# Optimization experiments

Measured on AMD Instinct MI355X. Metric: run time of the kernel, lower is better.

The kernel has to match this reference:

```python
import jax, jax.numpy as jnp
import numpy as np

B, S, T = 1024, 1024, 16


def setup_inputs() -> dict:
    key = jax.random.key(0)
    k1, k2, k3, k4, k5 = jax.random.split(key, 5)
    emissions = jax.random.normal(k1, (B, S, T), dtype=jnp.float32)
    tags = jax.random.randint(k2, (B, S), 0, T, dtype=jnp.int64)
    mask = jnp.ones((B, S), dtype=bool)
    # parameters (original uses uniform(-0.1, 0.1) init)
    transitions = jax.random.uniform(k3, (T, T), minval=-0.1, maxval=0.1, dtype=jnp.float32)
    start_transitions = jax.random.uniform(k4, (T,), minval=-0.1, maxval=0.1, dtype=jnp.float32)
    end_transitions = jax.random.uniform(k5, (T,), minval=-0.1, maxval=0.1, dtype=jnp.float32)
    return {
        "emissions": emissions,
        "tags": tags,
        "mask": mask,
        "transitions": transitions,
        "start_transitions": start_transitions,
        "end_transitions": end_transitions,
    }


def _forward_algorithm(emissions, mask, transitions, start_transitions, end_transitions):
    # emissions: [B,S,T], mask: [B,S] bool -> log partition [B]
    score0 = start_transitions + emissions[:, 0]  # [B,T]

    def step(score, xs):
        em_t, m_t = xs  # em_t: [B,T], m_t: [B]
        # next[b,i,j] = score[b,i] + transitions[i,j] + em_t[b,j]
        nxt = score[:, :, None] + transitions[None, :, :] + em_t[:, None, :]
        nxt = jax.nn.logsumexp(nxt, axis=1)  # over previous tag i
        score = jnp.where(m_t[:, None], nxt, score)
        return score, None

    em_rest = jnp.swapaxes(emissions[:, 1:], 0, 1)  # [S-1,B,T]
    m_rest = jnp.swapaxes(mask[:, 1:], 0, 1)        # [S-1,B]
    score, _ = jax.lax.scan(step, score0, (em_rest, m_rest))
    score = score + end_transitions
    return jax.nn.logsumexp(score, axis=1)


def _score_sentence(emissions, tags, mask, transitions, start_transitions, end_transitions):
    # gold-path score, vectorized over time. [B]
    bidx = jnp.arange(emissions.shape[0])
    score = start_transitions[tags[:, 0]] + emissions[:, 0][bidx, tags[:, 0]]
    # per-step emission scores [B,S]
    emit = jnp.take_along_axis(emissions, tags[:, :, None], axis=2)[:, :, 0]
    # NOTE: faithful to original: transitions[tags[t], tags[t-1]]
    trans = transitions[tags[:, 1:], tags[:, :-1]]  # [B,S-1]
    m = mask[:, 1:].astype(emissions.dtype)
    score = score + jnp.sum((emit[:, 1:] + trans) * m, axis=1)
    last_idx = jnp.sum(mask.astype(jnp.int32), axis=1) - 1  # [B]
    last_tags = jnp.take_along_axis(tags, last_idx[:, None].astype(tags.dtype), axis=1)[:, 0]
    score = score + end_transitions[last_tags]
    return score


def reference(emissions, tags, mask, transitions, start_transitions, end_transitions):
    emissions = emissions.astype(jnp.float32)
    gold = _score_sentence(emissions, tags, mask, transitions, start_transitions, end_transitions)
    logZ = _forward_algorithm(emissions, mask, transitions, start_transitions, end_transitions)
    nll = logZ - gold
    return jnp.mean(nll)
```

## Files before the change

### kernel.cpp

```cpp
#include <hip/hip_runtime.h>
#include <stdint.h>


#define BB 1024
#define SS 1024
#define TT 16
#define CC 16
#define LL 64
#define XS 68
#define P1B (BB * CC / 4)

typedef float    f32x4 __attribute__((ext_vector_type(4)));
typedef float    f32x2 __attribute__((ext_vector_type(2)));
typedef int      i32x4 __attribute__((ext_vector_type(4)));
typedef short    s16x4 __attribute__((ext_vector_type(4)));
typedef uint32_t u32x2 __attribute__((ext_vector_type(2)));

__device__ __forceinline__ uint32_t pkt(float lo, float hi) {
    return __builtin_amdgcn_perm(__float_as_uint(hi), __float_as_uint(lo), 0x07060302u);
}
__device__ __forceinline__ s16x4 mk_frag(uint32_t lo, uint32_t hi) {
    u32x2 t; t.x = lo; t.y = hi;
    return __builtin_bit_cast(s16x4, t);
}

__global__ __launch_bounds__(256, 4) void fused1_kernel(
        const float* __restrict__ em,
        const float* __restrict__ trans,
        const int*   __restrict__ tags,
        const float* __restrict__ startt,
        const float* __restrict__ endt,
        float* __restrict__ mats,
        int*   __restrict__ scales,
        float* __restrict__ gold,
        float* __restrict__ out)
{
    __shared__ float xbuf[4][TT * XS];
    __shared__ int   sbuf[4][16];
    __shared__ float red[256];
    if (blockIdx.x < P1B) {
        const int wave = threadIdx.x >> 6;
        const int lane = threadIdx.x & 63;
        const int id   = blockIdx.x * 4 + wave;
        const int b    = id >> 4;
        const int c    = id & 15;
        const int q    = lane >> 4;
        const int m    = lane & 15;

        const float comp = 1.00390625f;
        f32x2 e01, e23;
        e01.x = __expf(trans[(4*q + 0) * TT + m]) * comp;
        e01.y = __expf(trans[(4*q + 1) * TT + m]) * comp;
        e23.x = __expf(trans[(4*q + 2) * TT + m]) * comp;
        e23.y = __expf(trans[(4*q + 3) * TT + m]) * comp;

        const float* ep = em + (size_t)b * SS * TT + (size_t)c * LL * TT + lane;
        float* xb = xbuf[wave];
        {
            float v[16];
            #pragma unroll
            for (int k = 0; k < 16; ++k) v[k] = ep[k * 64];
            #pragma unroll
            for (int k = 0; k < 16; ++k) xb[m * XS + 4 * k + q] = __expf(v[k]);
        }

        f32x4 sd0, sd1;
        sd0[0] = sd1[0] = (4*q + 0 == m) ? 1.f : 0.f;
        sd0[1] = sd1[1] = (4*q + 1 == m) ? 1.f : 0.f;
        sd0[2] = sd1[2] = (4*q + 2 == m) ? 1.f : 0.f;
        sd0[3] = sd1[3] = (4*q + 3 == m) ? 1.f : 0.f;
        const f32x4 zero = {0.f, 0.f, 0.f, 0.f};
        int sc0 = 0, sc1 = 0;
        const bool skip0 = (c == 0);

#define RESCALE(sd, sc) {                                                   \
        float mx = fmaxf(fmaxf(sd[0], sd[1]), fmaxf(sd[2], sd[3]));         \
        mx = fmaxf(mx, __shfl_xor(mx, 16, 64));                             \
        mx = fmaxf(mx, __shfl_xor(mx, 32, 64));                             \
        const int e_ = (int)(__float_as_uint(mx) >> 23) - 127;              \
        const float sf_ = __uint_as_float((uint32_t)(127 - e_) << 23);      \
        sd[0] *= sf_; sd[1] *= sf_; sd[2] *= sf_; sd[3] *= sf_;             \
        sc += e_; }

#define STEP(sd, xm) {                                                      \
        f32x2 xx; xx.x = (xm); xx.y = (xm);                                 \
        const f32x2 a01 = xx * e01;                                         \
        const f32x2 a23 = xx * e23;                                         \
        const s16x4 afr = mk_frag(pkt(a01.x, a01.y), pkt(a23.x, a23.y));    \
        const s16x4 bfr = mk_frag(pkt(sd[0], sd[1]), pkt(sd[2], sd[3]));    \
        sd = __builtin_amdgcn_mfma_f32_16x16x16bf16_1k(afr, bfr, zero, 0, 0, 0); }

        const float* xrow = xb + m * XS;
        f32x4 cx0 = *(const f32x4*)(xrow);
        f32x4 cx1 = *(const f32x4*)(xrow + 32);

        #pragma unroll
        for (int g = 0; g < 8; ++g) {
            f32x4 nx0, nx1;
            if (g < 7) {
                nx0 = *(const f32x4*)(xrow + 4 * (g + 1));
                nx1 = *(const f32x4*)(xrow + 32 + 4 * (g + 1));
            }
            #pragma unroll
            for (int i = 0; i < 4; ++i) {
                if (!(skip0 && g == 0 && i == 0)) STEP(sd0, cx0[i]);
                STEP(sd1, cx1[i]);
            }
            if (g & 1) { RESCALE(sd0, sc0); RESCALE(sd1, sc1); }
            cx0 = nx0; cx1 = nx1;
        }

        xb[(4*q + 0) * TT + m] = sd1[0];
        xb[(4*q + 1) * TT + m] = sd1[1];
        xb[(4*q + 2) * TT + m] = sd1[2];
        xb[(4*q + 3) * TT + m] = sd1[3];
        if (q == 0) sbuf[wave][m] = sc1;
        const f32x4 at  = *(const f32x4*)(xb + m * TT + 4 * q);
        const i32x4 sh  = *(const i32x4*)(sbuf[wave] + 4 * q);
        int shimax = sc1;
        #pragma unroll
        for (int s = 1; s < 16; s <<= 1) shimax = max(shimax, __shfl_xor(shimax, s, 64));
        const float r0 = ldexpf(sd0[0], sh.x - shimax);
        const float r1 = ldexpf(sd0[1], sh.y - shimax);
        const float r2 = ldexpf(sd0[2], sh.z - shimax);
        const float r3 = ldexpf(sd0[3], sh.w - shimax);
        const s16x4 bfm = mk_frag(pkt(r0, r1), pkt(r2, r3));
        const s16x4 afm = mk_frag(pkt(at.x, at.y), pkt(at.z, at.w));
        f32x4 sd = __builtin_amdgcn_mfma_f32_16x16x16bf16_1k(afm, bfm, zero, 0, 0, 0);
        int sc = sc0 + shimax;
        RESCALE(sd, sc);
#undef RESCALE
#undef STEP

        float* mp = mats + (size_t)id * 256;
        mp[(4*q + 0) * TT + m] = sd[0];
        mp[(4*q + 1) * TT + m] = sd[1];
        mp[(4*q + 2) * TT + m] = sd[2];
        mp[(4*q + 3) * TT + m] = sd[3];
        if (q == 0) scales[id * 16 + m] = sc;
    } else {
        const int b = blockIdx.x - P1B, tid = threadIdx.x;
        if (b == 0 && tid == 0) out[0] = 0.f;
        float local = 0.f;
        for (int t = tid; t < SS; t += 256) {
            const int tg = tags[b * SS + t];
            float v = em[(size_t)(b * SS + t) * TT + tg];
            if (t > 0) v += trans[tg * TT + tags[b * SS + t - 1]];
            else       v += startt[tg];
            if (t == SS - 1) v += endt[tg];
            local += v;
        }
        red[tid] = local; __syncthreads();
        for (int s = 128; s > 0; s >>= 1) { if (tid < s) red[tid] += red[tid + s]; __syncthreads(); }
        if (tid == 0) gold[b] = red[0];
    }
}

__global__ __launch_bounds__(256) void combine_kernel(
        const float* __restrict__ em,
        const float* __restrict__ startt,
        const float* __restrict__ endt,
        const float* __restrict__ mats,
        const int*   __restrict__ scales,
        const float* __restrict__ gold,
        float* __restrict__ out)
{
    const int wave = threadIdx.x >> 6;
    const int lane = threadIdx.x & 63;
    const int b    = blockIdx.x * 4 + wave;
    const int q    = lane >> 4;
    const int m    = lane & 15;

    const float* m0 = mats + (size_t)(b * CC) * 256;
    f32x4 d;
    d[0] = m0[(4*q + 0) * TT + m];
    d[1] = m0[(4*q + 1) * TT + m];
    d[2] = m0[(4*q + 2) * TT + m];
    d[3] = m0[(4*q + 3) * TT + m];
    int sig = scales[(b * CC) * 16 + m];
    int gam = 0;
    const f32x4 zero = {0.f, 0.f, 0.f, 0.f};

    #pragma unroll 4
    for (int c = 1; c < CC; ++c) {
        const int idc = b * CC + c;
        const f32x4 a = *(const f32x4*)(mats + (size_t)idc * 256 + m * TT + 4 * q);
        const i32x4 s = *(const i32x4*)(scales + idc * 16 + 4 * q);
        int sm = max(max(s.x, s.y), max(s.z, s.w));
        sm = max(sm, __shfl_xor(sm, 16, 64));
        sm = max(sm, __shfl_xor(sm, 32, 64));
        const float r0 = ldexpf(d[0], s.x - sm);
        const float r1 = ldexpf(d[1], s.y - sm);
        const float r2 = ldexpf(d[2], s.z - sm);
        const float r3 = ldexpf(d[3], s.w - sm);
        const s16x4 bfr = mk_frag(pkt(r0, r1), pkt(r2, r3));
        const s16x4 afr = mk_frag(pkt(a.x, a.y), pkt(a.z, a.w));
        d = __builtin_amdgcn_mfma_f32_16x16x16bf16_1k(afr, bfr, zero, 0, 0, 0);
        gam += sm;
        float mx = fmaxf(fmaxf(d[0], d[1]), fmaxf(d[2], d[3]));
        mx = fmaxf(mx, __shfl_xor(mx, 16, 64));
        mx = fmaxf(mx, __shfl_xor(mx, 32, 64));
        const int e = (int)(__float_as_uint(mx) >> 23) - 127;
        const float sf = __uint_as_float((uint32_t)(127 - e) << 23);
        d[0] *= sf; d[1] *= sf; d[2] *= sf; d[3] *= sf;
        sig += e;
    }

    const float s0 = startt[m] + em[(size_t)b * SS * TT + m];
    float mx0 = s0;
    #pragma unroll
    for (int s = 1; s < 16; s <<= 1) mx0 = fmaxf(mx0, __shfl_xor(mx0, s, 64));
    const float u0n = __expf(s0 - mx0);

    int sigmax = sig;
    #pragma unroll
    for (int s = 1; s < 16; s <<= 1) sigmax = max(sigmax, __shfl_xor(sigmax, s, 64));
    const float w = ldexpf(u0n, sig - sigmax);

    f32x4 v;
    v[0] = d[0] * w; v[1] = d[1] * w; v[2] = d[2] * w; v[3] = d[3] * w;
    #pragma unroll
    for (int s = 1; s < 16; s <<= 1) {
        v[0] += __shfl_xor(v[0], s, 64);
        v[1] += __shfl_xor(v[1], s, 64);
        v[2] += __shfl_xor(v[2], s, 64);
        v[3] += __shfl_xor(v[3], s, 64);
    }
    const f32x4 ee = *(const f32x4*)(endt + 4 * q);
    float z = __expf(ee.x) * v[0] + __expf(ee.y) * v[1]
            + __expf(ee.z) * v[2] + __expf(ee.w) * v[3];
    z += __shfl_xor(z, 16, 64);
    z += __shfl_xor(z, 32, 64);

    if (lane == 0) {
        const float logZ = mx0 + 0.69314718055994531f * (float)(gam + sigmax) + __logf(z);
        atomicAdd(out, (logZ - gold[b]) * (1.0f / BB));
    }
}

extern "C" void kernel_launch(void* const* d_in, const int* in_sizes, int n_in,
                              void* d_out, int out_size, void* d_ws, size_t ws_size,
                              hipStream_t stream) {
    const float* em     = (const float*)d_in[0];
    const int*   tags   = (const int*)  d_in[1];
    const float* trans  = (const float*)d_in[3];
    const float* startt = (const float*)d_in[4];
    const float* endt   = (const float*)d_in[5];
    float* out = (float*)d_out;

    float* mats   = (float*)d_ws;
    int*   scales = (int*)((char*)d_ws + (size_t)BB * CC * 256 * 4);
    float* gold   = (float*)((char*)scales + (size_t)BB * CC * 16 * 4);

    fused1_kernel<<<P1B + BB, 256, 0, stream>>>(em, trans, tags, startt, endt, mats, scales, gold, out);
    combine_kernel<<<BB / 4, 256, 0, stream>>>(em, startt, endt, mats, scales, gold, out);
}
```

Baseline: 138.3 us.

## Fuse chunk products, gold score and combine into one block per sequence

Each block now handles one whole sequence with 8 waves, each wave covering 128 time steps as two 64-step chains. The per-wave 16x16 transfer matrices are merged in shared memory with a log-depth tree of MFMA products instead of being written to global memory and chained serially in a second kernel. The gold-path score is computed inside the same block with wave shuffles, and a tiny single-block reduction replaces the atomicAdd. This removes the global round trip of intermediate matrices and the serial 15-step combine, at the cost of longer per-wave chains and block-wide barriers.

```diff
diff --git a/kernel.cpp b/kernel.cpp
--- a/kernel.cpp
+++ b/kernel.cpp
@@ -5,10 +5,10 @@
 #define BB 1024
 #define SS 1024
 #define TT 16
-#define CC 16
-#define LL 64
-#define XS 68
-#define P1B (BB * CC / 4)
+#define WPB 8
+#define TL  128
+#define XS  132
+#define MS  20
 
 typedef float    f32x4 __attribute__((ext_vector_type(4)));
 typedef float    f32x2 __attribute__((ext_vector_type(2)));
@@ -24,54 +24,66 @@
     return __builtin_bit_cast(s16x4, t);
 }
 
-__global__ __launch_bounds__(256, 4) void fused1_kernel(
+__global__ __launch_bounds__(512, 4) void crf_fused(
         const float* __restrict__ em,
         const float* __restrict__ trans,
         const int*   __restrict__ tags,
         const float* __restrict__ startt,
         const float* __restrict__ endt,
-        float* __restrict__ mats,
-        int*   __restrict__ scales,
-        float* __restrict__ gold,
-        float* __restrict__ out)
+        float* __restrict__ part)
 {
-    __shared__ float xbuf[4][TT * XS];
-    __shared__ int   sbuf[4][16];
-    __shared__ float red[256];
-    if (blockIdx.x < P1B) {
-        const int wave = threadIdx.x >> 6;
-        const int lane = threadIdx.x & 63;
-        const int id   = blockIdx.x * 4 + wave;
-        const int b    = id >> 4;
-        const int c    = id & 15;
-        const int q    = lane >> 4;
-        const int m    = lane & 15;
-
-        const float comp = 1.00390625f;
-        f32x2 e01, e23;
-        e01.x = __expf(trans[(4*q + 0) * TT + m]) * comp;
-        e01.y = __expf(trans[(4*q + 1) * TT + m]) * comp;
-        e23.x = __expf(trans[(4*q + 2) * TT + m]) * comp;
-        e23.y = __expf(trans[(4*q + 3) * TT + m]) * comp;
-
-        const float* ep = em + (size_t)b * SS * TT + (size_t)c * LL * TT + lane;
-        float* xb = xbuf[wave];
-        {
-            float v[16];
-            #pragma unroll
-            for (int k = 0; k < 16; ++k) v[k] = ep[k * 64];
-            #pragma unroll
-            for (int k = 0; k < 16; ++k) xb[m * XS + 4 * k + q] = __expf(v[k]);
-        }
-
-        f32x4 sd0, sd1;
-        sd0[0] = sd1[0] = (4*q + 0 == m) ? 1.f : 0.f;
-        sd0[1] = sd1[1] = (4*q + 1 == m) ? 1.f : 0.f;
-        sd0[2] = sd1[2] = (4*q + 2 == m) ? 1.f : 0.f;
-        sd0[3] = sd1[3] = (4*q + 3 == m) ? 1.f : 0.f;
-        const f32x4 zero = {0.f, 0.f, 0.f, 0.f};
-        int sc0 = 0, sc1 = 0;
-        const bool skip0 = (c == 0);
+    __shared__ __align__(16) float xbuf[WPB][TT * XS];
+    __shared__ __align__(16) int   scb [WPB][16];
+    __shared__ float gpart[WPB];
+
+    const int w    = threadIdx.x >> 6;
+    const int lane = threadIdx.x & 63;
+    const int b    = blockIdx.x;
+    const int q    = lane >> 4;
+    const int m    = lane & 15;
+
+    const float comp = 1.00390625f;
+    f32x2 e01, e23;
+    e01.x = __expf(trans[(4*q + 0) * TT + m]) * comp;
+    e01.y = __expf(trans[(4*q + 1) * TT + m]) * comp;
+    e23.x = __expf(trans[(4*q + 2) * TT + m]) * comp;
+    e23.y = __expf(trans[(4*q + 3) * TT + m]) * comp;
+
+    const float* ep = em + (size_t)b * SS * TT + (size_t)w * TL * TT + lane;
+    float* xb = xbuf[w];
+    #pragma unroll
+    for (int h = 0; h < 2; ++h) {
+        float v[16];
+        #pragma unroll
+        for (int k = 0; k < 16; ++k) v[k] = ep[(h * 16 + k) * 64];
+        #pragma unroll
+        for (int k = 0; k < 16; ++k) xb[m * XS + 4 * (h * 16 + k) + q] = __expf(v[k]);
+    }
+
+    {
+        const int t0  = w * TL + lane;
+        const int t1  = t0 + 64;
+        const int tg0 = tags[b * SS + t0];
+        const int tg1 = tags[b * SS + t1];
+        float g0 = em[((size_t)b * SS + t0) * TT + tg0];
+        float g1 = em[((size_t)b * SS + t1) * TT + tg1];
+        g0 += (t0 > 0) ? trans[tg0 * TT + tags[b * SS + t0 - 1]] : startt[tg0];
+        g1 += trans[tg1 * TT + tags[b * SS + t1 - 1]];
+        if (t1 == SS - 1) g1 += endt[tg1];
+        float gs = g0 + g1;
+        #pragma unroll
+        for (int s2 = 1; s2 < 64; s2 <<= 1) gs += __shfl_xor(gs, s2, 64);
+        if (lane == 0) gpart[w] = gs;
+    }
+
+    f32x4 sd0, sd1;
+    sd0[0] = sd1[0] = (4*q + 0 == m) ? 1.f : 0.f;
+    sd0[1] = sd1[1] = (4*q + 1 == m) ? 1.f : 0.f;
+    sd0[2] = sd1[2] = (4*q + 2 == m) ? 1.f : 0.f;
+    sd0[3] = sd1[3] = (4*q + 3 == m) ? 1.f : 0.f;
+    const f32x4 zero = {0.f, 0.f, 0.f, 0.f};
+    int sc0 = 0, sc1 = 0;
+    const bool skip0 = (w == 0);
 
 #define RESCALE(sd, sc) {                                                   \
         float mx = fmaxf(fmaxf(sd[0], sd[1]), fmaxf(sd[2], sd[3]));         \
@@ -90,152 +102,143 @@
         const s16x4 bfr = mk_frag(pkt(sd[0], sd[1]), pkt(sd[2], sd[3]));    \
         sd = __builtin_amdgcn_mfma_f32_16x16x16bf16_1k(afr, bfr, zero, 0, 0, 0); }
 
-        const float* xrow = xb + m * XS;
-        f32x4 cx0 = *(const f32x4*)(xrow);
-        f32x4 cx1 = *(const f32x4*)(xrow + 32);
-
-        #pragma unroll
-        for (int g = 0; g < 8; ++g) {
-            f32x4 nx0, nx1;
-            if (g < 7) {
-                nx0 = *(const f32x4*)(xrow + 4 * (g + 1));
-                nx1 = *(const f32x4*)(xrow + 32 + 4 * (g + 1));
+    const float* xrow = xb + m * XS;
+    f32x4 cx0 = *(const f32x4*)(xrow);
+    f32x4 cx1 = *(const f32x4*)(xrow + 64);
+
+    #pragma unroll
+    for (int g = 0; g < 16; ++g) {
+        f32x4 nx0, nx1;
+        if (g < 15) {
+            nx0 = *(const f32x4*)(xrow + 4 * (g + 1));
+            nx1 = *(const f32x4*)(xrow + 64 + 4 * (g + 1));
+        }
+        #pragma unroll
+        for (int i = 0; i < 4; ++i) {
+            if (!(skip0 && g == 0 && i == 0)) STEP(sd0, cx0[i]);
+            STEP(sd1, cx1[i]);
+        }
+        if (g & 1) { RESCALE(sd0, sc0); RESCALE(sd1, sc1); }
+        cx0 = nx0; cx1 = nx1;
+    }
+
+    xb[(4*q + 0) * TT + m] = sd1[0];
+    xb[(4*q + 1) * TT + m] = sd1[1];
+    xb[(4*q + 2) * TT + m] = sd1[2];
+    xb[(4*q + 3) * TT + m] = sd1[3];
+    if (q == 0) scb[w][m] = sc1;
+    const f32x4 at = *(const f32x4*)(xb + m * TT + 4 * q);
+    const i32x4 sh = *(const i32x4*)(&scb[w][4 * q]);
+    int shimax = sc1;
+    #pragma unroll
+    for (int s2 = 1; s2 < 16; s2 <<= 1) shimax = max(shimax, __shfl_xor(shimax, s2, 64));
+    const float r0 = ldexpf(sd0[0], sh.x - shimax);
+    const float r1 = ldexpf(sd0[1], sh.y - shimax);
+    const float r2 = ldexpf(sd0[2], sh.z - shimax);
+    const float r3 = ldexpf(sd0[3], sh.w - shimax);
+    const s16x4 bfm = mk_frag(pkt(r0, r1), pkt(r2, r3));
+    const s16x4 afm = mk_frag(pkt(at.x, at.y), pkt(at.z, at.w));
+    f32x4 sdw = __builtin_amdgcn_mfma_f32_16x16x16bf16_1k(afm, bfm, zero, 0, 0, 0);
+    int scw = sc0 + shimax;
+    RESCALE(sdw, scw);
+
+    xb[(4*q + 0) * MS + m] = sdw[0];
+    xb[(4*q + 1) * MS + m] = sdw[1];
+    xb[(4*q + 2) * MS + m] = sdw[2];
+    xb[(4*q + 3) * MS + m] = sdw[3];
+    if (q == 0) scb[w][m] = scw;
+    __syncthreads();
+
+    f32x4 d = zero; int sig = 0;
+    #pragma unroll
+    for (int lev = 0; lev < 3; ++lev) {
+        const int nact = 4 >> lev;
+        if (w < nact) {
+            const int iA = (2 * w + 1) << lev;
+            const int iB = (2 * w) << lev;
+            const float* xA = xbuf[iA];
+            float*       xB = xbuf[iB];
+            const f32x4 a  = *(const f32x4*)(xA + m * MS + 4 * q);
+            const i32x4 s4 = *(const i32x4*)(&scb[iA][4 * q]);
+            const int   sB = scb[iB][m];
+            int smax = max(max(s4.x, s4.y), max(s4.z, s4.w));
+            smax = max(smax, __shfl_xor(smax, 16, 64));
+            smax = max(smax, __shfl_xor(smax, 32, 64));
+            const float bb0 = xB[(4*q + 0) * MS + m];
+            const float bb1 = xB[(4*q + 1) * MS + m];
+            const float bb2 = xB[(4*q + 2) * MS + m];
+            const float bb3 = xB[(4*q + 3) * MS + m];
+            const float u0 = ldexpf(bb0, s4.x - smax);
+            const float u1 = ldexpf(bb1, s4.y - smax);
+            const float u2 = ldexpf(bb2, s4.z - smax);
+            const float u3 = ldexpf(bb3, s4.w - smax);
+            const s16x4 bfr = mk_frag(pkt(u0, u1), pkt(u2, u3));
+            const s16x4 afr = mk_frag(pkt(a.x, a.y), pkt(a.z, a.w));
+            f32x4 dd = __builtin_amdgcn_mfma_f32_16x16x16bf16_1k(afr, bfr, zero, 0, 0, 0);
+            int sc_ = sB + smax;
+            RESCALE(dd, sc_);
+            if (lev == 2) { d = dd; sig = sc_; }
+            else {
+                xB[(4*q + 0) * MS + m] = dd[0];
+                xB[(4*q + 1) * MS + m] = dd[1];
+                xB[(4*q + 2) * MS + m] = dd[2];
+                xB[(4*q + 3) * MS + m] = dd[3];
+                if (q == 0) scb[iB][m] = sc_;
             }
-            #pragma unroll
-            for (int i = 0; i < 4; ++i) {
-                if (!(skip0 && g == 0 && i == 0)) STEP(sd0, cx0[i]);
-                STEP(sd1, cx1[i]);
-            }
-            if (g & 1) { RESCALE(sd0, sc0); RESCALE(sd1, sc1); }
-            cx0 = nx0; cx1 = nx1;
-        }
-
-        xb[(4*q + 0) * TT + m] = sd1[0];
-        xb[(4*q + 1) * TT + m] = sd1[1];
-        xb[(4*q + 2) * TT + m] = sd1[2];
-        xb[(4*q + 3) * TT + m] = sd1[3];
-        if (q == 0) sbuf[wave][m] = sc1;
-        const f32x4 at  = *(const f32x4*)(xb + m * TT + 4 * q);
-        const i32x4 sh  = *(const i32x4*)(sbuf[wave] + 4 * q);
-        int shimax = sc1;
-        #pragma unroll
-        for (int s = 1; s < 16; s <<= 1) shimax = max(shimax, __shfl_xor(shimax, s, 64));
-        const float r0 = ldexpf(sd0[0], sh.x - shimax);
-        const float r1 = ldexpf(sd0[1], sh.y - shimax);
-        const float r2 = ldexpf(sd0[2], sh.z - shimax);
-        const float r3 = ldexpf(sd0[3], sh.w - shimax);
-        const s16x4 bfm = mk_frag(pkt(r0, r1), pkt(r2, r3));
-        const s16x4 afm = mk_frag(pkt(at.x, at.y), pkt(at.z, at.w));
-        f32x4 sd = __builtin_amdgcn_mfma_f32_16x16x16bf16_1k(afm, bfm, zero, 0, 0, 0);
-        int sc = sc0 + shimax;
-        RESCALE(sd, sc);
+        }
+        if (lev < 2) __syncthreads();
+    }
 #undef RESCALE
 #undef STEP
 
-        float* mp = mats + (size_t)id * 256;
-        mp[(4*q + 0) * TT + m] = sd[0];
-        mp[(4*q + 1) * TT + m] = sd[1];
-        mp[(4*q + 2) * TT + m] = sd[2];
-        mp[(4*q + 3) * TT + m] = sd[3];
-        if (q == 0) scales[id * 16 + m] = sc;
-    } else {
-        const int b = blockIdx.x - P1B, tid = threadIdx.x;
-        if (b == 0 && tid == 0) out[0] = 0.f;
-        float local = 0.f;
-        for (int t = tid; t < SS; t += 256) {
-            const int tg = tags[b * SS + t];
-            float v = em[(size_t)(b * SS + t) * TT + tg];
-            if (t > 0) v += trans[tg * TT + tags[b * SS + t - 1]];
-            else       v += startt[tg];
-            if (t == SS - 1) v += endt[tg];
-            local += v;
-        }
-        red[tid] = local; __syncthreads();
-        for (int s = 128; s > 0; s >>= 1) { if (tid < s) red[tid] += red[tid + s]; __syncthreads(); }
-        if (tid == 0) gold[b] = red[0];
-    }
-}
-
-__global__ __launch_bounds__(256) void combine_kernel(
-        const float* __restrict__ em,
-        const float* __restrict__ startt,
-        const float* __restrict__ endt,
-        const float* __restrict__ mats,
-        const int*   __restrict__ scales,
-        const float* __restrict__ gold,
-        float* __restrict__ out)
+    if (w == 0) {
+        const float s0 = startt[m] + em[(size_t)b * SS * TT + m];
+        float mx0 = s0;
+        #pragma unroll
+        for (int s2 = 1; s2 < 16; s2 <<= 1) mx0 = fmaxf(mx0, __shfl_xor(mx0, s2, 64));
+        const float u0n = __expf(s0 - mx0);
+        int sigmax = sig;
+        #pragma unroll
+        for (int s2 = 1; s2 < 16; s2 <<= 1) sigmax = max(sigmax, __shfl_xor(sigmax, s2, 64));
+        const float wt = ldexpf(u0n, sig - sigmax);
+        f32x4 v;
+        v[0] = d[0] * wt; v[1] = d[1] * wt; v[2] = d[2] * wt; v[3] = d[3] * wt;
+        #pragma unroll
+        for (int s2 = 1; s2 < 16; s2 <<= 1) {
+            v[0] += __shfl_xor(v[0], s2, 64);
+            v[1] += __shfl_xor(v[1], s2, 64);
+            v[2] += __shfl_xor(v[2], s2, 64);
+            v[3] += __shfl_xor(v[3], s2, 64);
+        }
+        const f32x4 ee = *(const f32x4*)(endt + 4 * q);
+        float z = __expf(ee.x) * v[0] + __expf(ee.y) * v[1]
+                + __expf(ee.z) * v[2] + __expf(ee.w) * v[3];
+        z += __shfl_xor(z, 16, 64);
+        z += __shfl_xor(z, 32, 64);
+        if (lane == 0) {
+            float gb = 0.f;
+            #pragma unroll
+            for (int i = 0; i < WPB; ++i) gb += gpart[i];
+            part[b] = mx0 + 0.69314718055994531f * (float)sigmax + __logf(z) - gb;
+        }
+    }
+}
+
+__global__ __launch_bounds__(256) void reduce_kernel(const float* __restrict__ part,
+                                                     float* __restrict__ out)
 {
-    const int wave = threadIdx.x >> 6;
-    const int lane = threadIdx.x & 63;
-    const int b    = blockIdx.x * 4 + wave;
-    const int q    = lane >> 4;
-    const int m    = lane & 15;
-
-    const float* m0 = mats + (size_t)(b * CC) * 256;
-    f32x4 d;
-    d[0] = m0[(4*q + 0) * TT + m];
-    d[1] = m0[(4*q + 1) * TT + m];
-    d[2] = m0[(4*q + 2) * TT + m];
-    d[3] = m0[(4*q + 3) * TT + m];
-    int sig = scales[(b * CC) * 16 + m];
-    int gam = 0;
-    const f32x4 zero = {0.f, 0.f, 0.f, 0.f};
-
-    #pragma unroll 4
-    for (int c = 1; c < CC; ++c) {
-        const int idc = b * CC + c;
-        const f32x4 a = *(const f32x4*)(mats + (size_t)idc * 256 + m * TT + 4 * q);
-        const i32x4 s = *(const i32x4*)(scales + idc * 16 + 4 * q);
-        int sm = max(max(s.x, s.y), max(s.z, s.w));
-        sm = max(sm, __shfl_xor(sm, 16, 64));
-        sm = max(sm, __shfl_xor(sm, 32, 64));
-        const float r0 = ldexpf(d[0], s.x - sm);
-        const float r1 = ldexpf(d[1], s.y - sm);
-        const float r2 = ldexpf(d[2], s.z - sm);
-        const float r3 = ldexpf(d[3], s.w - sm);
-        const s16x4 bfr = mk_frag(pkt(r0, r1), pkt(r2, r3));
-        const s16x4 afr = mk_frag(pkt(a.x, a.y), pkt(a.z, a.w));
-        d = __builtin_amdgcn_mfma_f32_16x16x16bf16_1k(afr, bfr, zero, 0, 0, 0);
-        gam += sm;
-        float mx = fmaxf(fmaxf(d[0], d[1]), fmaxf(d[2], d[3]));
-        mx = fmaxf(mx, __shfl_xor(mx, 16, 64));
-        mx = fmaxf(mx, __shfl_xor(mx, 32, 64));
-        const int e = (int)(__float_as_uint(mx) >> 23) - 127;
-        const float sf = __uint_as_float((uint32_t)(127 - e) << 23);
-        d[0] *= sf; d[1] *= sf; d[2] *= sf; d[3] *= sf;
-        sig += e;
-    }
-
-    const float s0 = startt[m] + em[(size_t)b * SS * TT + m];
-    float mx0 = s0;
-    #pragma unroll
-    for (int s = 1; s < 16; s <<= 1) mx0 = fmaxf(mx0, __shfl_xor(mx0, s, 64));
-    const float u0n = __expf(s0 - mx0);
-
-    int sigmax = sig;
-    #pragma unroll
-    for (int s = 1; s < 16; s <<= 1) sigmax = max(sigmax, __shfl_xor(sigmax, s, 64));
-    const float w = ldexpf(u0n, sig - sigmax);
-
-    f32x4 v;
-    v[0] = d[0] * w; v[1] = d[1] * w; v[2] = d[2] * w; v[3] = d[3] * w;
-    #pragma unroll
-    for (int s = 1; s < 16; s <<= 1) {
-        v[0] += __shfl_xor(v[0], s, 64);
-        v[1] += __shfl_xor(v[1], s, 64);
-        v[2] += __shfl_xor(v[2], s, 64);
-        v[3] += __shfl_xor(v[3], s, 64);
-    }
-    const f32x4 ee = *(const f32x4*)(endt + 4 * q);
-    float z = __expf(ee.x) * v[0] + __expf(ee.y) * v[1]
-            + __expf(ee.z) * v[2] + __expf(ee.w) * v[3];
-    z += __shfl_xor(z, 16, 64);
-    z += __shfl_xor(z, 32, 64);
-
-    if (lane == 0) {
-        const float logZ = mx0 + 0.69314718055994531f * (float)(gam + sigmax) + __logf(z);
-        atomicAdd(out, (logZ - gold[b]) * (1.0f / BB));
-    }
+    __shared__ float red[256];
+    const int tid = threadIdx.x;
+    float s = 0.f;
+    #pragma unroll
+    for (int i = 0; i < 4; ++i) s += part[tid + 256 * i];
+    red[tid] = s;
+    __syncthreads();
+    for (int k = 128; k > 0; k >>= 1) {
+        if (tid < k) red[tid] += red[tid + k];
+        __syncthreads();
+    }
+    if (tid == 0) out[0] = red[0] * (1.0f / BB);
 }
 
 extern "C" void kernel_launch(void* const* d_in, const int* in_sizes, int n_in,
@@ -246,12 +249,9 @@
     const float* trans  = (const float*)d_in[3];
     const float* startt = (const float*)d_in[4];
     const float* endt   = (const float*)d_in[5];
-    float* out = (float*)d_out;
-
-    float* mats   = (float*)d_ws;
-    int*   scales = (int*)((char*)d_ws + (size_t)BB * CC * 256 * 4);
-    float* gold   = (float*)((char*)scales + (size_t)BB * CC * 16 * 4);
-
-    fused1_kernel<<<P1B + BB, 256, 0, stream>>>(em, trans, tags, startt, endt, mats, scales, gold, out);
-    combine_kernel<<<BB / 4, 256, 0, stream>>>(em, startt, endt, mats, scales, gold, out);
-}
+    float* out  = (float*)d_out;
+    float* part = (float*)d_ws;
+
+    crf_fused<<<BB, 512, 0, stream>>>(em, trans, tags, startt, endt, part);
+    reduce_kernel<<<1, 256, 0, stream>>>(part, out);
+}
```

Result: faster. 125.1 us (-9.6%).
